# Performance work log

Hardware: AMD Instinct MI355X
Metric: run time of the kernel (lower is better)

## Reference

```python
import jax, jax.numpy as jnp
import numpy as np

D_HEAD = 64
D_ATTN = 64


def setup_inputs() -> dict:
    key = jax.random.key(0)
    ks = jax.random.split(key, 6)
    B, H, T = 2, 8, 512
    q = jax.random.normal(ks[0], (B, H, T, D_HEAD), dtype=jnp.float32)
    k = jax.random.normal(ks[1], (B, H, T, D_HEAD), dtype=jnp.float32)
    v = jax.random.normal(ks[2], (B, H, T, D_HEAD), dtype=jnp.float32)
    mask = jnp.ones((B, H, T, T), dtype=bool)
    # learned params (nn.Linear(d_head, d_attn, bias=False) stores weight [d_attn, d_head])
    Wq = jax.random.normal(ks[3], (D_ATTN, D_HEAD), dtype=jnp.float32) / np.sqrt(D_HEAD)
    Wk = jax.random.normal(ks[4], (D_ATTN, D_HEAD), dtype=jnp.float32) / np.sqrt(D_HEAD)
    Wv = jax.random.normal(ks[5], (D_ATTN,), dtype=jnp.float32) / np.sqrt(D_ATTN)  # Linear(d_attn,1)
    return {"q": q, "k": k, "v": v, "mask": mask, "Wq": Wq, "Wk": Wk, "Wv": Wv}


def reference(q, k, v, mask, Wq, Wk, Wv):
    # q_proj: [B,H,Tq,d_attn], k_proj: [B,H,Tk,d_attn]
    q_proj = jnp.einsum('bhqd,ad->bhqa', q, Wq)
    k_proj = jnp.einsum('bhkd,ad->bhka', k, Wk)
    # broadcast add -> tanh -> contract with v-vector: [B,H,Tq,Tk]
    scores = jnp.einsum('bhqka,a->bhqk',
                        jnp.tanh(q_proj[:, :, :, None, :] + k_proj[:, :, None, :, :]),
                        Wv)
    scores = jnp.where(mask, scores, -1e9)
    attn = jax.nn.softmax(scores, axis=-1)
    # dropout is identity in eval mode
    out = jnp.einsum('bhqk,bhkd->bhqd', attn, v)
    return (out, attn)
```

## Files before the change

kernel.cpp:

```cpp
#include <hip/hip_runtime.h>
#include <stddef.h>


#define LOG2E 1.4426950408889634f

__global__ __launch_bounds__(256) void proj_kernel(
    const float* __restrict__ Q, const float* __restrict__ K,
    const float* __restrict__ Wq, const float* __restrict__ Wk,
    float* __restrict__ Eq, float* __restrict__ Ek)
{
    __shared__ __align__(16) float wlds[64][68];
    __shared__ __align__(16) float xlds[8][64];
    const int tid = threadIdx.x;
    const bool isK = blockIdx.x >= 1024;
    const int r0 = (isK ? (blockIdx.x - 1024) : blockIdx.x) * 8;
    const float* X = isK ? K : Q;
    const float* W = isK ? Wk : Wq;
    float* E = isK ? Ek : Eq;

    for (int i = tid; i < 4096; i += 256) wlds[i >> 6][i & 63] = W[i];
    if (tid < 128)
        ((float4*)xlds)[tid] = ((const float4*)(X + (size_t)r0 * 64))[tid];
    __syncthreads();

    const int a   = tid & 63;
    const int row = tid >> 6;
    float acc0 = 0.f, acc1 = 0.f;
#pragma unroll
    for (int d4 = 0; d4 < 16; ++d4) {
        const float4 w4 = *(const float4*)&wlds[a][d4 * 4];
        const float4 x0 = *(const float4*)&xlds[row][d4 * 4];
        const float4 x1 = *(const float4*)&xlds[row + 4][d4 * 4];
        acc0 = fmaf(x0.x, w4.x, acc0); acc0 = fmaf(x0.y, w4.y, acc0);
        acc0 = fmaf(x0.z, w4.z, acc0); acc0 = fmaf(x0.w, w4.w, acc0);
        acc1 = fmaf(x1.x, w4.x, acc1); acc1 = fmaf(x1.y, w4.y, acc1);
        acc1 = fmaf(x1.z, w4.z, acc1); acc1 = fmaf(x1.w, w4.w, acc1);
    }
    E[(size_t)(r0 + row) * 64 + a]     = __builtin_amdgcn_exp2f(acc0 * (2.f * LOG2E));
    E[(size_t)(r0 + row + 4) * 64 + a] = __builtin_amdgcn_exp2f(acc1 * (2.f * LOG2E));
}

__global__ __launch_bounds__(512, 8) void attn_kernel(
    const float* __restrict__ Eq, const float* __restrict__ Ek,
    const float* __restrict__ Wv, const float* __restrict__ V,
    float* __restrict__ out, float* __restrict__ attn)
{
    __shared__ __align__(16) float ekbuf[2][64 * 68];
    float (*p_lds)[512] = (float(*)[512])&ekbuf[0][0];

    const int tid  = threadIdx.x;
    const int bh   = blockIdx.x >> 6;
    const int q0   = (blockIdx.x & 63) * 8;
    const int lane = tid & 63;
    const int wu   = __builtin_amdgcn_readfirstlane(tid >> 6);

    const float* __restrict__ eqr = Eq + (size_t)(bh * 512 + q0 + wu) * 64;
    const float* ekg = Ek + (size_t)bh * 32768;

    const int f4a = tid, f4b = 512 + tid;
    const int da = (f4a >> 4) * 68 + (f4a & 15) * 4;
    const int db = (f4b >> 4) * 68 + (f4b & 15) * 4;

    {
        const float4* src = (const float4*)ekg;
        *(float4*)&ekbuf[0][da] = src[f4a];
        *(float4*)&ekbuf[0][db] = src[f4b];
    }
    __syncthreads();

    float sc[8];
#pragma unroll
    for (int kt = 0; kt < 8; ++kt) {
        const float* ekl = &ekbuf[kt & 1][lane * 68];

        float4 st0, st1;
        if (kt < 7) {
            const float4* src = (const float4*)(ekg + (kt + 1) * 4096);
            st0 = src[f4a];
            st1 = src[f4b];
        }

        float acc = 0.f;
#pragma unroll
        for (int a4 = 0; a4 < 16; ++a4) {
            const float4 ek = *(const float4*)&ekl[a4 * 4];
            const float4 g  = *(const float4*)&eqr[a4 * 4];
            const float4 wv = *(const float4*)&Wv[a4 * 4];
            const float D0 = fmaf(g.x, ek.x, 1.f);
            const float D1 = fmaf(g.y, ek.y, 1.f);
            const float D2 = fmaf(g.z, ek.z, 1.f);
            const float D3 = fmaf(g.w, ek.w, 1.f);
            const float d01 = D0 * D1, d23 = D2 * D3;
            const float n01 = fmaf(wv.x, D1, wv.y * D0);
            const float n23 = fmaf(wv.z, D3, wv.w * D2);
            const float num = fmaf(n01, d23, n23 * d01);
            acc = fmaf(num, __builtin_amdgcn_rcpf(d01 * d23), acc);
        }
        sc[kt] = acc;

        if (kt < 7) {
            float* dst = &ekbuf[(kt + 1) & 1][0];
            *(float4*)&dst[da] = st0;
            *(float4*)&dst[db] = st1;
            __syncthreads();
        }
    }

    float C = 0.f;
#pragma unroll
    for (int i = 0; i < 64; ++i) C += Wv[i];
#pragma unroll
    for (int t = 0; t < 8; ++t) sc[t] = fmaf(-2.f, sc[t], C);

    {
        float m = sc[0];
#pragma unroll
        for (int t = 1; t < 8; ++t) m = fmaxf(m, sc[t]);
#pragma unroll
        for (int off = 32; off >= 1; off >>= 1) m = fmaxf(m, __shfl_xor(m, off));

        float e[8], sum = 0.f;
#pragma unroll
        for (int t = 0; t < 8; ++t) {
            e[t] = __builtin_amdgcn_exp2f((sc[t] - m) * LOG2E);
            sum += e[t];
        }
#pragma unroll
        for (int off = 32; off >= 1; off >>= 1) sum += __shfl_xor(sum, off);

        const float rinv = __builtin_amdgcn_rcpf(sum);
        float* ar = attn + ((size_t)(bh * 512 + q0 + wu)) * 512;
#pragma unroll
        for (int t = 0; t < 8; ++t) {
            const float p = e[t] * rinv;
            p_lds[wu][lane + 64 * t] = p;
            ar[lane + 64 * t] = p;
        }
    }
    __syncthreads();

    {
        const float* vbase = V + (size_t)bh * 32768 + lane;
        float o = 0.f;
#pragma unroll 8
        for (int k4 = 0; k4 < 128; ++k4) {
            const float4 p = *(const float4*)&p_lds[wu][4 * k4];
            o = fmaf(p.x, vbase[(4 * k4 + 0) * 64], o);
            o = fmaf(p.y, vbase[(4 * k4 + 1) * 64], o);
            o = fmaf(p.z, vbase[(4 * k4 + 2) * 64], o);
            o = fmaf(p.w, vbase[(4 * k4 + 3) * 64], o);
        }
        out[((size_t)(bh * 512 + q0 + wu)) * 64 + lane] = o;
    }
}

extern "C" void kernel_launch(void* const* d_in, const int* in_sizes, int n_in,
                              void* d_out, int out_size, void* d_ws, size_t ws_size,
                              hipStream_t stream) {
    const float* q  = (const float*)d_in[0];
    const float* k  = (const float*)d_in[1];
    const float* v  = (const float*)d_in[2];
    const float* Wq = (const float*)d_in[4];
    const float* Wk = (const float*)d_in[5];
    const float* Wv = (const float*)d_in[6];

    float* out  = (float*)d_out;
    float* attn = (float*)d_out + (size_t)2 * 8 * 512 * 64;

    float* eqw = (float*)d_ws;
    float* ekw = eqw + (size_t)8192 * 64;

    proj_kernel<<<2048, 256, 0, stream>>>(q, k, Wq, Wk, eqw, ekw);
    attn_kernel<<<1024, 512, 0, stream>>>(eqw, ekw, Wv, v, out, attn);
}
```

Measured before the change: 156.7 us.

## Split PV over keys per wave, hoist Eq/Wv into registers, remap blocks

The P·V stage now has each wave handle a 64-key slice for all 8 query rows, then reduces the partial sums through LDS. Before, every wave streamed the whole V tile for its own row, so V was read from global/L2 eight times per block; now each V element is read once per block. Eq rows and Wv are preloaded into registers, with Wv made wave-uniform through readfirstlane so it can sit in scalar registers. The score loop splits its accumulator in two to shorten the dependency chain. The block-to-(bh,q) mapping is reordered and occupancy is lowered to 4 blocks per CU to allow the larger register footprint, which costs latency hiding.

```diff
diff --git a/kernel.cpp b/kernel.cpp
--- a/kernel.cpp
+++ b/kernel.cpp
@@ -3,6 +3,11 @@
 
 
 #define LOG2E 1.4426950408889634f
+
+__device__ __forceinline__ float rfl_f32(float x) {
+    return __builtin_bit_cast(float,
+        __builtin_amdgcn_readfirstlane(__builtin_bit_cast(int, x)));
+}
 
 __global__ __launch_bounds__(256) void proj_kernel(
     const float* __restrict__ Q, const float* __restrict__ K,
@@ -40,27 +45,46 @@
     E[(size_t)(r0 + row + 4) * 64 + a] = __builtin_amdgcn_exp2f(acc1 * (2.f * LOG2E));
 }
 
-__global__ __launch_bounds__(512, 8) void attn_kernel(
+__global__ __launch_bounds__(512, 4) void attn_kernel(
     const float* __restrict__ Eq, const float* __restrict__ Ek,
     const float* __restrict__ Wv, const float* __restrict__ V,
     float* __restrict__ out, float* __restrict__ attn)
 {
-    __shared__ __align__(16) float ekbuf[2][64 * 68];
+    __shared__ __align__(16) float ekbuf[2][4352];
     float (*p_lds)[512] = (float(*)[512])&ekbuf[0][0];
+    float* part = &ekbuf[1][0];
 
     const int tid  = threadIdx.x;
-    const int bh   = blockIdx.x >> 6;
-    const int q0   = (blockIdx.x & 63) * 8;
+    const int bx   = blockIdx.x;
+    const int bh   = ((bx & 7) << 1) | ((bx >> 3) & 1);
+    const int q0   = (bx >> 4) * 8;
     const int lane = tid & 63;
     const int wu   = __builtin_amdgcn_readfirstlane(tid >> 6);
 
-    const float* __restrict__ eqr = Eq + (size_t)(bh * 512 + q0 + wu) * 64;
+    float wvs[64];
+#pragma unroll
+    for (int i = 0; i < 16; ++i) {
+        const float4 t = ((const float4*)Wv)[i];
+        wvs[4 * i + 0] = rfl_f32(t.x);
+        wvs[4 * i + 1] = rfl_f32(t.y);
+        wvs[4 * i + 2] = rfl_f32(t.z);
+        wvs[4 * i + 3] = rfl_f32(t.w);
+    }
+    float C = 0.f;
+#pragma unroll
+    for (int i = 0; i < 64; ++i) C += wvs[i];
+
+    float4 g4[16];
+    {
+        const float4* eqr = (const float4*)(Eq + (size_t)(bh * 512 + q0 + wu) * 64);
+#pragma unroll
+        for (int i = 0; i < 16; ++i) g4[i] = eqr[i];
+    }
+
     const float* ekg = Ek + (size_t)bh * 32768;
-
-    const int f4a = tid, f4b = 512 + tid;
+    const int f4a = tid, f4b = tid + 512;
     const int da = (f4a >> 4) * 68 + (f4a & 15) * 4;
     const int db = (f4b >> 4) * 68 + (f4b & 15) * 4;
-
     {
         const float4* src = (const float4*)ekg;
         *(float4*)&ekbuf[0][da] = src[f4a];
@@ -80,23 +104,24 @@
             st1 = src[f4b];
         }
 
-        float acc = 0.f;
+        float accA = 0.f, accB = 0.f;
 #pragma unroll
         for (int a4 = 0; a4 < 16; ++a4) {
             const float4 ek = *(const float4*)&ekl[a4 * 4];
-            const float4 g  = *(const float4*)&eqr[a4 * 4];
-            const float4 wv = *(const float4*)&Wv[a4 * 4];
+            const float4 g  = g4[a4];
             const float D0 = fmaf(g.x, ek.x, 1.f);
             const float D1 = fmaf(g.y, ek.y, 1.f);
             const float D2 = fmaf(g.z, ek.z, 1.f);
             const float D3 = fmaf(g.w, ek.w, 1.f);
             const float d01 = D0 * D1, d23 = D2 * D3;
-            const float n01 = fmaf(wv.x, D1, wv.y * D0);
-            const float n23 = fmaf(wv.z, D3, wv.w * D2);
+            const float n01 = fmaf(wvs[4 * a4 + 0], D1, wvs[4 * a4 + 1] * D0);
+            const float n23 = fmaf(wvs[4 * a4 + 2], D3, wvs[4 * a4 + 3] * D2);
             const float num = fmaf(n01, d23, n23 * d01);
-            acc = fmaf(num, __builtin_amdgcn_rcpf(d01 * d23), acc);
-        }
-        sc[kt] = acc;
+            const float r   = __builtin_amdgcn_rcpf(d01 * d23);
+            if (a4 & 1) accB = fmaf(num, r, accB);
+            else        accA = fmaf(num, r, accA);
+        }
+        sc[kt] = accA + accB;
 
         if (kt < 7) {
             float* dst = &ekbuf[(kt + 1) & 1][0];
@@ -105,10 +130,6 @@
             __syncthreads();
         }
     }
-
-    float C = 0.f;
-#pragma unroll
-    for (int i = 0; i < 64; ++i) C += Wv[i];
 #pragma unroll
     for (int t = 0; t < 8; ++t) sc[t] = fmaf(-2.f, sc[t], C);
 
@@ -140,17 +161,37 @@
     __syncthreads();
 
     {
-        const float* vbase = V + (size_t)bh * 32768 + lane;
+        float acc8[8] = {0.f, 0.f, 0.f, 0.f, 0.f, 0.f, 0.f, 0.f};
+        const float* vb = V + (size_t)bh * 32768 + lane;
+        const int kk0 = wu * 64;
+#pragma unroll
+        for (int k4 = 0; k4 < 16; ++k4) {
+            const int kk = kk0 + 4 * k4;
+            const float v0 = vb[(kk + 0) * 64];
+            const float v1 = vb[(kk + 1) * 64];
+            const float v2 = vb[(kk + 2) * 64];
+            const float v3 = vb[(kk + 3) * 64];
+#pragma unroll
+            for (int r = 0; r < 8; ++r) {
+                const float4 p = *(const float4*)&p_lds[r][kk];
+                acc8[r] = fmaf(p.x, v0, acc8[r]);
+                acc8[r] = fmaf(p.y, v1, acc8[r]);
+                acc8[r] = fmaf(p.z, v2, acc8[r]);
+                acc8[r] = fmaf(p.w, v3, acc8[r]);
+            }
+        }
+#pragma unroll
+        for (int r = 0; r < 8; ++r)
+            part[wu * 512 + r * 64 + lane] = acc8[r];
+    }
+    __syncthreads();
+
+    {
+        const int r = tid >> 6;
         float o = 0.f;
-#pragma unroll 8
-        for (int k4 = 0; k4 < 128; ++k4) {
-            const float4 p = *(const float4*)&p_lds[wu][4 * k4];
-            o = fmaf(p.x, vbase[(4 * k4 + 0) * 64], o);
-            o = fmaf(p.y, vbase[(4 * k4 + 1) * 64], o);
-            o = fmaf(p.z, vbase[(4 * k4 + 2) * 64], o);
-            o = fmaf(p.w, vbase[(4 * k4 + 3) * 64], o);
-        }
-        out[((size_t)(bh * 512 + q0 + wu)) * 64 + lane] = o;
+#pragma unroll
+        for (int w2 = 0; w2 < 8; ++w2) o += part[w2 * 512 + r * 64 + lane];
+        out[((size_t)(bh * 512 + q0 + r)) * 64 + lane] = o;
     }
 }
 
```

After: 423.6 us. +170.3%, slower.
